# Kernel optimization log

Hardware: AMD Instinct MI355X
Metric: run time of the kernel (lower is better)

The kernel has to match this reference:

```python
import jax, jax.numpy as jnp
import numpy as np

NUM_CLASSES = 19
EPS = 1e-05


def setup_inputs() -> dict:
    key = jax.random.key(0)
    k1, k2 = jax.random.split(key)
    y_pred = jax.random.normal(k1, (16, NUM_CLASSES, 512, 512), dtype=jnp.float32)
    y = jax.random.randint(k2, (16, 512, 512), 0, NUM_CLASSES, dtype=jnp.int64)
    return {"y_pred": y_pred, "y": y}


def reference(y_pred, y):
    C = NUM_CLASSES
    # hard predictions: [B, H, W]
    pred = jnp.argmax(y_pred, axis=1)
    y_flat = y.reshape(-1).astype(jnp.int32)
    pred_flat = pred.reshape(-1).astype(jnp.int32)
    # single-pass confusion-matrix histogram instead of per-class loop
    pair = y_flat * C + pred_flat                     # [N]
    cm = jnp.bincount(pair, length=C * C).reshape(C, C).astype(jnp.float32)
    inter = jnp.diagonal(cm)                           # |y==i & pred==i|
    count_y = cm.sum(axis=1)                           # |y==i|
    count_p = cm.sum(axis=0)                           # |pred==i|
    union = count_y + count_p - inter                  # |y==i | pred==i|
    dice = (2.0 * inter + EPS) / (union + EPS)         # [C]
    return (jnp.float32(1.0) - jnp.mean(dice)).astype(jnp.float32)
```

## Files before the change

kernel.cpp:

```cpp
#include <hip/hip_runtime.h>

#define NCLS 19
#define CM_BINS (NCLS * NCLS)
#define EPS 1e-5f
#define HW 262144
#define HW4 65536

typedef float f32x4 __attribute__((ext_vector_type(4)));
typedef int   i32x4 __attribute__((ext_vector_type(4)));

__global__ void __launch_bounds__(256)
dice_cm_kernel(const float* __restrict__ y_pred,
               const int* __restrict__ y,
               unsigned int* __restrict__ cm,
               int n_vec) {
    __shared__ unsigned int s_cm[CM_BINS];
    const int tid = threadIdx.x;
    for (int i = tid; i < CM_BINS; i += 256) s_cm[i] = 0u;
    __syncthreads();

    for (int pv = blockIdx.x * 256 + tid; pv < n_vec; pv += gridDim.x * 256) {
        const int b   = pv >> 16;
        const int hw4 = pv & 65535;
        const float* p = y_pred + (size_t)b * ((size_t)NCLS * HW) + (size_t)hw4 * 4;

        f32x4 best = __builtin_nontemporal_load(reinterpret_cast<const f32x4*>(p));
        int bcx = 0, bcy = 0, bcz = 0, bcw = 0;
        #pragma unroll
        for (int c = 1; c < NCLS; ++c) {
            f32x4 v = __builtin_nontemporal_load(
                reinterpret_cast<const f32x4*>(p + (size_t)c * HW));
            if (v.x > best.x) { best.x = v.x; bcx = c; }
            if (v.y > best.y) { best.y = v.y; bcy = c; }
            if (v.z > best.z) { best.z = v.z; bcz = c; }
            if (v.w > best.w) { best.w = v.w; bcw = c; }
        }

        const i32x4 lab = __builtin_nontemporal_load(
            reinterpret_cast<const i32x4*>(y + (size_t)pv * 4));

        atomicAdd(&s_cm[lab.x * NCLS + bcx], 1u);
        atomicAdd(&s_cm[lab.y * NCLS + bcy], 1u);
        atomicAdd(&s_cm[lab.z * NCLS + bcz], 1u);
        atomicAdd(&s_cm[lab.w * NCLS + bcw], 1u);
    }

    __syncthreads();
    for (int i = tid; i < CM_BINS; i += 256) {
        const unsigned int v = s_cm[i];
        if (v) atomicAdd(&cm[i], v);
    }
}

__global__ void dice_finalize(const unsigned int* __restrict__ cm,
                              float* __restrict__ out) {
    const int lane = threadIdx.x;
    float d = 0.0f;
    if (lane < NCLS) {
        float cy = 0.0f, cp = 0.0f;
        #pragma unroll
        for (int j = 0; j < NCLS; ++j) {
            cy += (float)cm[lane * NCLS + j];
            cp += (float)cm[j * NCLS + lane];
        }
        const float inter = (float)cm[lane * NCLS + lane];
        const float uni   = cy + cp - inter;
        d = (2.0f * inter + EPS) / (uni + EPS);
    }
    #pragma unroll
    for (int off = 32; off > 0; off >>= 1) d += __shfl_down(d, off);
    if (lane == 0) out[0] = 1.0f - d * (1.0f / (float)NCLS);
}

extern "C" void kernel_launch(void* const* d_in, const int* in_sizes, int n_in,
                              void* d_out, int out_size, void* d_ws, size_t ws_size,
                              hipStream_t stream) {
    const float* y_pred = (const float*)d_in[0];
    const int*   y      = (const int*)d_in[1];
    float*       out    = (float*)d_out;
    unsigned int* cm    = (unsigned int*)d_ws;

    hipMemsetAsync(cm, 0, CM_BINS * sizeof(unsigned int), stream);

    const int n_pix = in_sizes[1];
    const int n_vec = n_pix / 4;

    const int block = 256;
    const int grid  = 2048;
    dice_cm_kernel<<<grid, block, 0, stream>>>(y_pred, y, cm, n_vec);
    dice_finalize<<<1, 64, 0, stream>>>(cm, out);
}
```

Before: 76.67 us.

## Fuse dice finalize into histogram kernel via last-block ticket, batch loads

Removes the separate finalize kernel launch by having the last block (found through an atomic ticket counter in the workspace) reduce the confusion matrix and write the dice loss. Class loads are grouped four at a time, with the label load moved ahead of them, to raise memory-level parallelism. Launch bounds now request 6 waves per EU. This adds a threadfence, an extra global atomic per block, and a counter that must be zeroed by the memset.

```diff
diff --git a/kernel.cpp b/kernel.cpp
--- a/kernel.cpp
+++ b/kernel.cpp
@@ -4,40 +4,68 @@
 #define CM_BINS (NCLS * NCLS)
 #define EPS 1e-5f
 #define HW 262144
-#define HW4 65536
+#define BLOCK 256
+#define GRID 2048
 
 typedef float f32x4 __attribute__((ext_vector_type(4)));
 typedef int   i32x4 __attribute__((ext_vector_type(4)));
 
-__global__ void __launch_bounds__(256)
+#define NTLOAD(ptr) __builtin_nontemporal_load(reinterpret_cast<const f32x4*>(ptr))
+
+#define CMP1(c, v)                                          \
+    do {                                                    \
+        if ((v).x > best.x) { best.x = (v).x; bcx = (c); }  \
+        if ((v).y > best.y) { best.y = (v).y; bcy = (c); }  \
+        if ((v).z > best.z) { best.z = (v).z; bcz = (c); }  \
+        if ((v).w > best.w) { best.w = (v).w; bcw = (c); }  \
+    } while (0)
+
+__global__ void __launch_bounds__(BLOCK, 6)
 dice_cm_kernel(const float* __restrict__ y_pred,
                const int* __restrict__ y,
-               unsigned int* __restrict__ cm,
+               unsigned int* __restrict__ ws,
+               float* __restrict__ out,
                int n_vec) {
     __shared__ unsigned int s_cm[CM_BINS];
+    __shared__ unsigned int s_last;
     const int tid = threadIdx.x;
-    for (int i = tid; i < CM_BINS; i += 256) s_cm[i] = 0u;
+    for (int i = tid; i < CM_BINS; i += BLOCK) s_cm[i] = 0u;
     __syncthreads();
 
-    for (int pv = blockIdx.x * 256 + tid; pv < n_vec; pv += gridDim.x * 256) {
+    for (int pv = blockIdx.x * BLOCK + tid; pv < n_vec; pv += GRID * BLOCK) {
         const int b   = pv >> 16;
         const int hw4 = pv & 65535;
         const float* p = y_pred + (size_t)b * ((size_t)NCLS * HW) + (size_t)hw4 * 4;
 
-        f32x4 best = __builtin_nontemporal_load(reinterpret_cast<const f32x4*>(p));
+        const i32x4 lab = __builtin_nontemporal_load(
+            reinterpret_cast<const i32x4*>(y) + pv);
+
+        f32x4 best = NTLOAD(p);
         int bcx = 0, bcy = 0, bcz = 0, bcw = 0;
-        #pragma unroll
-        for (int c = 1; c < NCLS; ++c) {
-            f32x4 v = __builtin_nontemporal_load(
-                reinterpret_cast<const f32x4*>(p + (size_t)c * HW));
-            if (v.x > best.x) { best.x = v.x; bcx = c; }
-            if (v.y > best.y) { best.y = v.y; bcy = c; }
-            if (v.z > best.z) { best.z = v.z; bcz = c; }
-            if (v.w > best.w) { best.w = v.w; bcw = c; }
+        {
+            f32x4 a = NTLOAD(p + 1 * (size_t)HW), b2 = NTLOAD(p + 2 * (size_t)HW),
+                  c = NTLOAD(p + 3 * (size_t)HW), d = NTLOAD(p + 4 * (size_t)HW);
+            CMP1(1, a); CMP1(2, b2); CMP1(3, c); CMP1(4, d);
         }
-
-        const i32x4 lab = __builtin_nontemporal_load(
-            reinterpret_cast<const i32x4*>(y + (size_t)pv * 4));
+        {
+            f32x4 a = NTLOAD(p + 5 * (size_t)HW), b2 = NTLOAD(p + 6 * (size_t)HW),
+                  c = NTLOAD(p + 7 * (size_t)HW), d = NTLOAD(p + 8 * (size_t)HW);
+            CMP1(5, a); CMP1(6, b2); CMP1(7, c); CMP1(8, d);
+        }
+        {
+            f32x4 a = NTLOAD(p + 9 * (size_t)HW), b2 = NTLOAD(p + 10 * (size_t)HW),
+                  c = NTLOAD(p + 11 * (size_t)HW), d = NTLOAD(p + 12 * (size_t)HW);
+            CMP1(9, a); CMP1(10, b2); CMP1(11, c); CMP1(12, d);
+        }
+        {
+            f32x4 a = NTLOAD(p + 13 * (size_t)HW), b2 = NTLOAD(p + 14 * (size_t)HW),
+                  c = NTLOAD(p + 15 * (size_t)HW), d = NTLOAD(p + 16 * (size_t)HW);
+            CMP1(13, a); CMP1(14, b2); CMP1(15, c); CMP1(16, d);
+        }
+        {
+            f32x4 a = NTLOAD(p + 17 * (size_t)HW), b2 = NTLOAD(p + 18 * (size_t)HW);
+            CMP1(17, a); CMP1(18, b2);
+        }
 
         atomicAdd(&s_cm[lab.x * NCLS + bcx], 1u);
         atomicAdd(&s_cm[lab.y * NCLS + bcy], 1u);
@@ -46,30 +74,39 @@
     }
 
     __syncthreads();
-    for (int i = tid; i < CM_BINS; i += 256) {
+    for (int i = tid; i < CM_BINS; i += BLOCK) {
         const unsigned int v = s_cm[i];
-        if (v) atomicAdd(&cm[i], v);
+        if (v) atomicAdd(&ws[i], v);
     }
-}
+    __syncthreads();
 
-__global__ void dice_finalize(const unsigned int* __restrict__ cm,
-                              float* __restrict__ out) {
-    const int lane = threadIdx.x;
-    float d = 0.0f;
-    if (lane < NCLS) {
-        float cy = 0.0f, cp = 0.0f;
-        #pragma unroll
-        for (int j = 0; j < NCLS; ++j) {
-            cy += (float)cm[lane * NCLS + j];
-            cp += (float)cm[j * NCLS + lane];
+    if (tid == 0) {
+        __threadfence();
+        s_last = (atomicAdd(&ws[CM_BINS], 1u) == GRID - 1) ? 1u : 0u;
+    }
+    __syncthreads();
+
+    if (s_last) {
+        for (int i = tid; i < CM_BINS; i += BLOCK)
+            s_cm[i] = atomicAdd(&ws[i], 0u);
+        __syncthreads();
+        if (tid < 64) {
+            float d = 0.0f;
+            if (tid < NCLS) {
+                float cy = 0.0f, cp = 0.0f;
+                #pragma unroll
+                for (int j = 0; j < NCLS; ++j) {
+                    cy += (float)s_cm[tid * NCLS + j];
+                    cp += (float)s_cm[j * NCLS + tid];
+                }
+                const float inter = (float)s_cm[tid * NCLS + tid];
+                d = (2.0f * inter + EPS) / (cy + cp - inter + EPS);
+            }
+            #pragma unroll
+            for (int off = 32; off > 0; off >>= 1) d += __shfl_down(d, off);
+            if (tid == 0) out[0] = 1.0f - d * (1.0f / (float)NCLS);
         }
-        const float inter = (float)cm[lane * NCLS + lane];
-        const float uni   = cy + cp - inter;
-        d = (2.0f * inter + EPS) / (uni + EPS);
     }
-    #pragma unroll
-    for (int off = 32; off > 0; off >>= 1) d += __shfl_down(d, off);
-    if (lane == 0) out[0] = 1.0f - d * (1.0f / (float)NCLS);
 }
 
 extern "C" void kernel_launch(void* const* d_in, const int* in_sizes, int n_in,
@@ -78,15 +115,12 @@
     const float* y_pred = (const float*)d_in[0];
     const int*   y      = (const int*)d_in[1];
     float*       out    = (float*)d_out;
-    unsigned int* cm    = (unsigned int*)d_ws;
+    unsigned int* ws    = (unsigned int*)d_ws;
 
-    hipMemsetAsync(cm, 0, CM_BINS * sizeof(unsigned int), stream);
+    hipMemsetAsync(ws, 0, (CM_BINS + 1) * sizeof(unsigned int), stream);
 
     const int n_pix = in_sizes[1];
     const int n_vec = n_pix / 4;
 
-    const int block = 256;
-    const int grid  = 2048;
-    dice_cm_kernel<<<grid, block, 0, stream>>>(y_pred, y, cm, n_vec);
-    dice_finalize<<<1, 64, 0, stream>>>(cm, out);
+    dice_cm_kernel<<<GRID, BLOCK, 0, stream>>>(y_pred, y, ws, out, n_vec);
 }
```

Result: slower. 160.0 us (+108.6%).
